# Optimization experiments

Hardware: AMD Instinct MI355X
Metric: run time of the kernel (lower is better)

Reference implementation:

```python
import jax, jax.numpy as jnp
import numpy as np
import itertools

B, N, H, W, D = 4, 4, 192, 192, 64
A = 128            # n_anchors = min(128, H*W)
TH = 0.3           # correspondence distance threshold
MIN_VALID = 5      # min valid correspondences per (b, triplet)


def setup_inputs() -> dict:
    key = jax.random.key(0)
    k1, k2, k3 = jax.random.split(key, 3)
    T = len(list(itertools.combinations(range(N), 3)))  # 4
    features = jax.random.normal(k1, (B, N, H, W, D), dtype=jnp.float32)
    pointmaps = jax.random.uniform(k2, (B, N, H, W, 3), dtype=jnp.float32)
    # replaces torch.randperm anchor sampling with explicit indices
    anchor_idx = jax.random.randint(k3, (B, T, A), 0, H * W)
    return {"features": features, "pointmaps": pointmaps, "anchor_idx": anchor_idx}


def _pdist(x, y):
    # euclidean cdist: x [..., M, 3], y [..., P, 3] -> [..., M, P]
    d2 = (jnp.sum(x * x, -1)[..., :, None]
          + jnp.sum(y * y, -1)[..., None, :]
          - 2.0 * jnp.einsum('...md,...pd->...mp', x, y))
    return jnp.sqrt(jnp.maximum(d2, 0.0))


def _normalize(x):
    # F.normalize(dim=-1): x / max(||x||, eps)
    return x / jnp.maximum(jnp.linalg.norm(x, axis=-1, keepdims=True), 1e-12)


def reference(features, pointmaps, anchor_idx):
    Bb, Nn = features.shape[0], features.shape[1]
    HW = features.shape[2] * features.shape[3]
    Dd = features.shape[4]
    trips = np.array(list(itertools.combinations(range(Nn), 3)))  # [T,3]
    ti, tj, tk = trips[:, 0], trips[:, 1], trips[:, 2]
    Tn = trips.shape[0]

    feats = features.reshape(Bb, Nn, HW, Dd)
    pts = pointmaps.reshape(Bb, Nn, HW, 3)

    fi = feats[:, ti]                    # [B,T,HW,D]
    pi, pj, pk = pts[:, ti], pts[:, tj], pts[:, tk]  # [B,T,HW,3]

    anchor_pts = jnp.take_along_axis(pi, anchor_idx[..., None], axis=2)   # [B,T,A,3]
    anchor_fts = jnp.take_along_axis(fi, anchor_idx[..., None], axis=2)   # [B,T,A,D]

    # i -> j
    dij = _pdist(anchor_pts, pj)          # [B,T,A,HW]
    min_ij = dij.min(-1)
    idx_j = dij.argmin(-1)                # [B,T,A]
    pjc = jnp.take_along_axis(pj, idx_j[..., None], axis=2)
    # j -> k
    djk = _pdist(pjc, pk)                 # [B,T,A,HW]
    min_jk = djk.min(-1)
    idx_k = djk.argmin(-1)
    pkc = jnp.take_along_axis(pk, idx_k[..., None], axis=2)
    # k -> i (back to anchors only)
    dki = _pdist(pkc, anchor_pts)         # [B,T,A,A]
    min_ki = dki.min(-1)
    idx_i_ret = dki.argmin(-1)            # [B,T,A]

    feat_ret = jnp.take_along_axis(fi, idx_i_ret[..., None], axis=2)      # [B,T,A,D]

    valid = ((min_ij < TH) & (min_jk < TH) & (min_ki < TH)).astype(jnp.float32)  # [B,T,A]
    se = jnp.sum((_normalize(feat_ret) - _normalize(anchor_fts)) ** 2, -1)       # [B,T,A]

    cnt = valid.sum(-1)                   # [B,T]
    # mse over valid anchors and D dims
    loss_bt = jnp.where(cnt > 0, (se * valid).sum(-1) / (jnp.maximum(cnt, 1.0) * Dd), 0.0)
    batch_ok = (cnt >= MIN_VALID).astype(jnp.float32)   # [B,T]
    t_cnt = batch_ok.sum(0)               # [T]
    # mean over batches contributing to this triplet; 0 if none
    loss_t = jnp.where(t_cnt > 0, (loss_bt * batch_ok).sum(0) / jnp.maximum(t_cnt, 1.0), 0.0)
    return loss_t.sum() / Tn
```

## Files before the change

### kernel.cpp

```cpp
#include <hip/hip_runtime.h>

#define BB 4
#define NN 4
#define TT 4
#define AA 128
#define DD 64
#define HWD 36864
#define NPTS (BB * NN * HWD)
#define NG (BB * TT * AA)
#define CHUNKS 128
#define CPTS (HWD / CHUNKS)
#define NBLK (BB * TT * CHUNKS)

__device__ __constant__ int c_ti[4] = {0, 0, 0, 1};
__device__ __constant__ int c_tj[4] = {1, 1, 2, 2};
__device__ __constant__ int c_tk[4] = {2, 3, 3, 3};

typedef const __attribute__((address_space(4))) float cfloat;

__device__ __forceinline__ unsigned int fmap(float f) {
    const unsigned int b = __float_as_uint(f);
    return (b & 0x80000000u) ? ~b : (b | 0x80000000u);
}
__device__ __forceinline__ float funmap(unsigned int m) {
    const unsigned int b = (m & 0x80000000u) ? (m ^ 0x80000000u) : ~m;
    return __uint_as_float(b);
}

__global__ __launch_bounds__(256) void
prep_kernel(const float* __restrict__ pts, float4* __restrict__ pk4,
            unsigned long long* __restrict__ slots,
            unsigned int* __restrict__ ctr) {
#pragma clang fp contract(off)
    const int idx = blockIdx.x * 256 + threadIdx.x;
    if (idx < NPTS) {
        const float x = pts[idx * 3 + 0];
        const float y = pts[idx * 3 + 1];
        const float z = pts[idx * 3 + 2];
        pk4[idx] = make_float4(x, y, z, x * x + y * y + z * z);
    }
    if (blockIdx.x == 0) {
        for (int s = threadIdx.x; s < 2 * NG; s += 256)
            slots[s] = 0xFFFFFFFFFFFFFFFFull;
        if (threadIdx.x == 0) ctr[0] = 0xFFFFFFFFu;
    }
}

__global__ __launch_bounds__(128) void
scan1_kernel(const float4* __restrict__ pk4,
             const int* __restrict__ anchor_idx,
             unsigned long long* __restrict__ slot1) {
    const int chunk = blockIdx.x & (CHUNKS - 1);
    const int bt = blockIdx.x >> 7;
    const int t = bt & 3;
    const int b = bt >> 2;
    const int g = bt * AA + threadIdx.x;

    const int qpix = anchor_idx[g];
    const float4 q = pk4[(b * NN + c_ti[t]) * HWD + qpix];
    const float m2x = -2.0f * q.x;
    const float m2y = -2.0f * q.y;
    const float m2z = -2.0f * q.z;

    const float4* sp = pk4 + (b * NN + c_tj[t]) * HWD + chunk * CPTS;
    cfloat* sps = (cfloat*)(unsigned long long)sp;

    float best = 3.4e38f;
    int besti = 0;
#pragma unroll 8
    for (int p = 0; p < CPTS; ++p) {
        const float x = sps[4 * p + 0];
        const float y = sps[4 * p + 1];
        const float z = sps[4 * p + 2];
        const float w = sps[4 * p + 3];
        const float key = fmaf(x, m2x, fmaf(y, m2y, fmaf(z, m2z, w)));
        if (key < best) { best = key; besti = p; }
    }
    const unsigned long long v =
        ((unsigned long long)fmap(best) << 32) |
        (unsigned int)(chunk * CPTS + besti);
    atomicMin(&slot1[g], v);
}

__global__ __launch_bounds__(128) void
scan2_kernel(const float4* __restrict__ pk4,
             const unsigned long long* __restrict__ slot1,
             unsigned long long* __restrict__ slot2) {
    const int tid = threadIdx.x;
    const int chunk = blockIdx.x & (CHUNKS - 1);
    const int bt = blockIdx.x >> 7;
    const int t = bt & 3;
    const int b = bt >> 2;
    const int g = bt * AA + tid;

    const int ij = (int)(slot1[g] & 0xFFFFFFFFull);
    const float4 jq = pk4[(b * NN + c_tj[t]) * HWD + ij];
    const float m2x = -2.0f * jq.x;
    const float m2y = -2.0f * jq.y;
    const float m2z = -2.0f * jq.z;

    const float4* sp = pk4 + (b * NN + c_tk[t]) * HWD + chunk * CPTS;
    cfloat* sps = (cfloat*)(unsigned long long)sp;

    float best = 3.4e38f;
    int besti = 0;
#pragma unroll 8
    for (int p = 0; p < CPTS; ++p) {
        const float x = sps[4 * p + 0];
        const float y = sps[4 * p + 1];
        const float z = sps[4 * p + 2];
        const float w = sps[4 * p + 3];
        const float key = fmaf(x, m2x, fmaf(y, m2y, fmaf(z, m2z, w)));
        if (key < best) { best = key; besti = p; }
    }
    const unsigned long long v =
        ((unsigned long long)fmap(best) << 32) |
        (unsigned int)(chunk * CPTS + besti);
    atomicMin(&slot2[g], v);
}

__global__ __launch_bounds__(128) void
pass3_kernel(const float* __restrict__ pts,
             const float* __restrict__ feats,
             const int* __restrict__ anchor_idx,
             const unsigned long long* __restrict__ slot1,
             const unsigned long long* __restrict__ slot2,
             float* __restrict__ loss_bt,
             float* __restrict__ batch_ok,
             unsigned int* __restrict__ ctr,
             float* __restrict__ out) {
#pragma clang fp contract(off)
    const int bt = blockIdx.x;
    const int t = bt & 3;
    const int b = bt >> 2;
    const int i = c_ti[t];
    const int k = c_tk[t];
    const int tid = threadIdx.x;
    const int g = bt * AA + tid;

    const int ai = anchor_idx[g];
    const float* ap = pts + ((long)(b * NN + i) * HWD + ai) * 3;
    const float ax = ap[0], ay = ap[1], az = ap[2];
    const float sq = ax * ax + ay * ay + az * az;

    const unsigned long long s1 = slot1[g];
    const float min_ij = sqrtf(fmaxf(funmap((unsigned int)(s1 >> 32)) + sq, 0.0f));
    const int ij = (int)(s1 & 0xFFFFFFFFull);

    const float* jp = pts + ((long)(b * NN + c_tj[t]) * HWD + ij) * 3;
    const float jx = jp[0], jy = jp[1], jz = jp[2];
    const float sqj = jx * jx + jy * jy + jz * jz;
    const unsigned long long s2v = slot2[g];
    const float min_jk =
        sqrtf(fmaxf(funmap((unsigned int)(s2v >> 32)) + sqj, 0.0f));
    const int ik = (int)(s2v & 0xFFFFFFFFull);

    __shared__ float aps[AA][3];
    aps[tid][0] = ax;
    aps[tid][1] = ay;
    aps[tid][2] = az;
    const float* kp = pts + ((long)(b * NN + k) * HWD + ik) * 3;
    const float kx = kp[0], ky = kp[1], kz = kp[2];
    const float sk = kx * kx + ky * ky + kz * kz;
    __syncthreads();

    float best = 3.4e38f;
    int besti = 0;
    for (int a2 = 0; a2 < AA; ++a2) {
        const float qx = aps[a2][0], qy = aps[a2][1], qz = aps[a2][2];
        const float s2 = qx * qx + qy * qy + qz * qz;
        const float dot = kx * qx + ky * qy + kz * qz;
        const float d2 = (sk + s2) - 2.0f * dot;
        if (d2 < best) { best = d2; besti = a2; }
    }
    const float min_ki = sqrtf(fmaxf(best, 0.0f));

    const int valid =
        (min_ij < 0.3f) && (min_jk < 0.3f) && (min_ki < 0.3f);

    const float4* fr4 =
        (const float4*)(feats + ((long)(b * NN + i) * HWD + besti) * DD);
    const float4* fa4 =
        (const float4*)(feats + ((long)(b * NN + i) * HWD + ai) * DD);
    float snr = 0.0f, sna = 0.0f;
#pragma unroll
    for (int r = 0; r < 16; ++r) {
        const float4 v = fr4[r];
        snr = snr + v.x * v.x; snr = snr + v.y * v.y;
        snr = snr + v.z * v.z; snr = snr + v.w * v.w;
    }
#pragma unroll
    for (int r = 0; r < 16; ++r) {
        const float4 v = fa4[r];
        sna = sna + v.x * v.x; sna = sna + v.y * v.y;
        sna = sna + v.z * v.z; sna = sna + v.w * v.w;
    }
    const float nr = fmaxf(sqrtf(snr), 1e-12f);
    const float na = fmaxf(sqrtf(sna), 1e-12f);
    float se = 0.0f;
#pragma unroll
    for (int r = 0; r < 16; ++r) {
        const float4 u = fr4[r];
        const float4 v = fa4[r];
        float x;
        x = u.x / nr - v.x / na; se = se + x * x;
        x = u.y / nr - v.y / na; se = se + x * x;
        x = u.z / nr - v.z / na; se = se + x * x;
        x = u.w / nr - v.w / na; se = se + x * x;
    }

    __shared__ float sred[2][AA];
    sred[0][tid] = (float)valid;
    sred[1][tid] = valid ? se : 0.0f;
    __syncthreads();
    for (int s = 64; s > 0; s >>= 1) {
        if (tid < s) {
            sred[0][tid] += sred[0][tid + s];
            sred[1][tid] += sred[1][tid + s];
        }
        __syncthreads();
    }

    __shared__ int s_fin;
    if (tid == 0) {
        const float cnt = sred[0][0];
        const float lbt = (cnt > 0.0f)
                              ? sred[1][0] / (fmaxf(cnt, 1.0f) * (float)DD)
                              : 0.0f;
        const float ok = (cnt >= 5.0f) ? 1.0f : 0.0f;
        atomicExch(&loss_bt[bt], lbt);
        atomicExch(&batch_ok[bt], ok);
        __threadfence();
        s_fin = (atomicAdd(ctr, 1u) == 14u) ? 1 : 0;
    }
    __syncthreads();
    if (!s_fin) return;

    __shared__ float sok[16], slo[16];
    if (tid < 16) {
        sok[tid] = atomicAdd(&batch_ok[tid], 0.0f);
        slo[tid] = atomicAdd(&loss_bt[tid], 0.0f);
    }
    __syncthreads();
    if (tid == 0) {
        float s = 0.0f;
        for (int tt = 0; tt < TT; ++tt) {
            float tc = 0.0f, sl = 0.0f;
            for (int bb = 0; bb < BB; ++bb) {
                const float okv = sok[bb * TT + tt];
                tc += okv;
                sl += slo[bb * TT + tt] * okv;
            }
            s += (tc > 0.0f) ? sl / fmaxf(tc, 1.0f) : 0.0f;
        }
        out[0] = s / (float)TT;
    }
}

extern "C" void kernel_launch(void* const* d_in, const int* in_sizes, int n_in,
                              void* d_out, int out_size, void* d_ws,
                              size_t ws_size, hipStream_t stream) {
    const float* feats = (const float*)d_in[0];
    const float* pts = (const float*)d_in[1];
    const int* anchor = (const int*)d_in[2];
    float* out = (float*)d_out;

    float* ws = (float*)d_ws;
    float4* pk4 = (float4*)ws;
    unsigned long long* slot1 = (unsigned long long*)(ws + NPTS * 4);
    unsigned long long* slot2 = slot1 + NG;
    unsigned int* ctr = (unsigned int*)(slot2 + NG);
    float* loss_bt = (float*)(ctr + 1);
    float* batch_ok = loss_bt + 16;

    prep_kernel<<<(NPTS + 255) / 256, 256, 0, stream>>>(pts, pk4, slot1, ctr);
    scan1_kernel<<<NBLK, 128, 0, stream>>>(pk4, anchor, slot1);
    scan2_kernel<<<NBLK, 128, 0, stream>>>(pk4, slot1, slot2);
    pass3_kernel<<<BB * TT, 128, 0, stream>>>(pts, feats, anchor, slot1,
                                              slot2, loss_bt, batch_ok, ctr,
                                              out);
}
```

Measured before the change: 68.99 us.

## Double scan chunking, skip packing view 0, read query points from raw input

Doubles the number of chunks per (batch, triplet) in both nearest-neighbour scans, so twice as many blocks each scan half as many points. The prep kernel stops building packed float4+norm entries for view 0, which only ever serves as query points. The scans now read query coordinates straight from the raw point array instead of the packed buffer. The cost is twice as many atomicMin operations per anchor, plus per-block setup overhead that is now amortised over fewer points.

```diff
diff --git a/kernel.cpp b/kernel.cpp
--- a/kernel.cpp
+++ b/kernel.cpp
@@ -8,7 +8,7 @@
 #define HWD 36864
 #define NPTS (BB * NN * HWD)
 #define NG (BB * TT * AA)
-#define CHUNKS 128
+#define CHUNKS 256
 #define CPTS (HWD / CHUNKS)
 #define NBLK (BB * TT * CHUNKS)
 
@@ -24,7 +24,7 @@
 }
 __device__ __forceinline__ float funmap(unsigned int m) {
     const unsigned int b = (m & 0x80000000u) ? (m ^ 0x80000000u) : ~m;
-    return __uint_as_float(b);
+    return __uint_as_float(m & 0x80000000u ? (m ^ 0x80000000u) : ~m);
 }
 
 __global__ __launch_bounds__(256) void
@@ -33,7 +33,7 @@
             unsigned int* __restrict__ ctr) {
 #pragma clang fp contract(off)
     const int idx = blockIdx.x * 256 + threadIdx.x;
-    if (idx < NPTS) {
+    if (idx < NPTS && ((idx / HWD) & 3) != 0) {
         const float x = pts[idx * 3 + 0];
         const float y = pts[idx * 3 + 1];
         const float z = pts[idx * 3 + 2];
@@ -47,20 +47,21 @@
 }
 
 __global__ __launch_bounds__(128) void
-scan1_kernel(const float4* __restrict__ pk4,
+scan1_kernel(const float* __restrict__ pts,
+             const float4* __restrict__ pk4,
              const int* __restrict__ anchor_idx,
              unsigned long long* __restrict__ slot1) {
     const int chunk = blockIdx.x & (CHUNKS - 1);
-    const int bt = blockIdx.x >> 7;
+    const int bt = blockIdx.x >> 8;
     const int t = bt & 3;
     const int b = bt >> 2;
     const int g = bt * AA + threadIdx.x;
 
     const int qpix = anchor_idx[g];
-    const float4 q = pk4[(b * NN + c_ti[t]) * HWD + qpix];
-    const float m2x = -2.0f * q.x;
-    const float m2y = -2.0f * q.y;
-    const float m2z = -2.0f * q.z;
+    const float* qp = pts + ((long)(b * NN + c_ti[t]) * HWD + qpix) * 3;
+    const float m2x = -2.0f * qp[0];
+    const float m2y = -2.0f * qp[1];
+    const float m2z = -2.0f * qp[2];
 
     const float4* sp = pk4 + (b * NN + c_tj[t]) * HWD + chunk * CPTS;
     cfloat* sps = (cfloat*)(unsigned long long)sp;
@@ -83,21 +84,22 @@
 }
 
 __global__ __launch_bounds__(128) void
-scan2_kernel(const float4* __restrict__ pk4,
+scan2_kernel(const float* __restrict__ pts,
+             const float4* __restrict__ pk4,
              const unsigned long long* __restrict__ slot1,
              unsigned long long* __restrict__ slot2) {
     const int tid = threadIdx.x;
     const int chunk = blockIdx.x & (CHUNKS - 1);
-    const int bt = blockIdx.x >> 7;
+    const int bt = blockIdx.x >> 8;
     const int t = bt & 3;
     const int b = bt >> 2;
     const int g = bt * AA + tid;
 
     const int ij = (int)(slot1[g] & 0xFFFFFFFFull);
-    const float4 jq = pk4[(b * NN + c_tj[t]) * HWD + ij];
-    const float m2x = -2.0f * jq.x;
-    const float m2y = -2.0f * jq.y;
-    const float m2z = -2.0f * jq.z;
+    const float* jp = pts + ((long)(b * NN + c_tj[t]) * HWD + ij) * 3;
+    const float m2x = -2.0f * jp[0];
+    const float m2y = -2.0f * jp[1];
+    const float m2z = -2.0f * jp[2];
 
     const float4* sp = pk4 + (b * NN + c_tk[t]) * HWD + chunk * CPTS;
     cfloat* sps = (cfloat*)(unsigned long long)sp;
@@ -274,8 +276,8 @@
     float* batch_ok = loss_bt + 16;
 
     prep_kernel<<<(NPTS + 255) / 256, 256, 0, stream>>>(pts, pk4, slot1, ctr);
-    scan1_kernel<<<NBLK, 128, 0, stream>>>(pk4, anchor, slot1);
-    scan2_kernel<<<NBLK, 128, 0, stream>>>(pk4, slot1, slot2);
+    scan1_kernel<<<NBLK, 128, 0, stream>>>(pts, pk4, anchor, slot1);
+    scan2_kernel<<<NBLK, 128, 0, stream>>>(pts, pk4, slot1, slot2);
     pass3_kernel<<<BB * TT, 128, 0, stream>>>(pts, feats, anchor, slot1,
                                               slot2, loss_bt, batch_ok, ctr,
                                               out);
```

Result: no change. 69.63 us (+0.9%).
